# Kernel tuning notes

Hardware: AMD Instinct MI355X
Metric: run time of the kernel (lower is better)

The kernel has to match this reference:

```python
import jax, jax.numpy as jnp
import numpy as np

B, S, D, H = 4, 4096, 1024, 1024


def log_g(x):
    # where(x >= 0, log(relu(x) + 0.5), -softplus(-x)); relu(x)+0.5 >= 0.5 so log is safe
    return jnp.where(x >= 0, jnp.log(jax.nn.relu(x) + 0.5), -jax.nn.softplus(-x))


def setup_inputs() -> dict:
    key = jax.random.key(0)
    ks = jax.random.split(key, 8)
    scale = 1.0 / np.sqrt(D)
    return {
        "x_t": jax.random.normal(ks[0], (B, S, D), dtype=jnp.float32),
        "pre_h": jax.random.normal(ks[1], (B, 1, H), dtype=jnp.float32),
        "W_f": jax.random.uniform(ks[2], (H, D), jnp.float32, -scale, scale),
        "b_f": jax.random.uniform(ks[3], (H,), jnp.float32, -scale, scale),
        "W_i": jax.random.uniform(ks[4], (H, D), jnp.float32, -scale, scale),
        "b_i": jax.random.uniform(ks[5], (H,), jnp.float32, -scale, scale),
        "W_h": jax.random.uniform(ks[6], (H, D), jnp.float32, -scale, scale),
        "b_h": jax.random.uniform(ks[7], (H,), jnp.float32, -scale, scale),
    }


def reference(x_t, pre_h, W_f, b_f, W_i, b_i, W_h, b_h):
    sp = jax.nn.softplus
    f_pre = jnp.einsum("bsd,hd->bsh", x_t, W_f) + b_f
    i_pre = jnp.einsum("bsd,hd->bsh", x_t, W_i) + b_i
    h_pre = jnp.einsum("bsd,hd->bsh", x_t, W_h) + b_h

    diff = sp(-f_pre) - sp(-i_pre)
    log_f = -sp(diff)        # (B, S, H)
    log_i = -sp(-diff)       # (B, S, H)

    log_h0 = log_g(pre_h)                 # (B, 1, H)
    log_tilde_h = log_g(h_pre)            # (B, S, H)
    log_values = jnp.concatenate([log_h0, log_i + log_tilde_h], axis=1)  # (B, S+1, H)

    # parallel_scan_log: pad cumsum at END of seq dim (as in source: F.pad(..., (0,0,0,1)))
    a_star = jnp.pad(jnp.cumsum(log_f, axis=1), ((0, 0), (0, 1), (0, 0)))  # (B, S+1, H)
    log_h0_plus_b_star = jax.lax.cumlogsumexp(log_values - a_star, axis=1)
    log_h = a_star + log_h0_plus_b_star
    return jnp.exp(log_h)[:, 1:]  # (B, S, H)
```

## Files before the change

kernel.cpp:

```cpp
#include <hip/hip_runtime.h>
#include <hip/hip_bf16.h>
#include <math.h>

#define B_DIM 4
#define S_DIM 4096
#define K_DIM 1024
#define H_DIM 1024
#define M_DIM (B_DIM * S_DIM)

#define BMT 128
#define BNT 128
#define KT_ITERS (K_DIM / 32)

#define NCHUNK 64
#define CLEN (S_DIM / NCHUNK)

typedef __attribute__((ext_vector_type(8))) _Float16 f16x8;
typedef __attribute__((ext_vector_type(4))) _Float16 f16x4;
typedef __attribute__((ext_vector_type(4))) float f32x4;

__device__ __forceinline__ float sp_f(float x) {
    return fmaxf(x, 0.0f) + __logf(1.0f + __expf(-fabsf(x)));
}
__device__ __forceinline__ float log_g_f(float x) {
    return (x >= 0.0f) ? __logf(x + 0.5f) : -sp_f(-x);
}
__device__ __forceinline__ float logaddexp_f(float a, float b) {
    float m = fmaxf(a, b);
    return m + __logf(1.0f + __expf(-fabsf(a - b)));
}
__device__ __forceinline__ float exp_sat(float x) {
    return __expf(fminf(x, 85.0f));
}

__device__ __forceinline__ void gl_lds16(const void* g, void* l) {
    __builtin_amdgcn_global_load_lds(
        (const __attribute__((address_space(1))) unsigned int*)g,
        (__attribute__((address_space(3))) unsigned int*)l, 16, 0, 0);
}

__global__ __launch_bounds__(256) void conv_f16(
    const float* __restrict__ src, _Float16* __restrict__ dst, int n4)
{
    int i = blockIdx.x * 256 + threadIdx.x;
    if (i >= n4) return;
    float4 v = ((const float4*)src)[i];
    f16x4 o = {(_Float16)v.x, (_Float16)v.y, (_Float16)v.z, (_Float16)v.w};
    ((f16x4*)dst)[i] = o;
}

__global__ __launch_bounds__(512, 2) void gemm3(
    const _Float16* __restrict__ xh,
    const _Float16* __restrict__ wh,
    const float* __restrict__ bfp, const float* __restrict__ bip,
    const float* __restrict__ bhp,
    _Float16* __restrict__ lf_out, _Float16* __restrict__ w_out)
{
    __shared__ __align__(16) char smem0[32768];
    __shared__ __align__(16) char smem1[32768];
    __shared__ __align__(16) char smem2[32768];

    const int tid = threadIdx.x;
    const int lane = tid & 63;
    const int wv = tid >> 6;
    const int wm = wv >> 2;
    const int wn = wv & 3;

    const int row0 = blockIdx.y * BMT;
    const int col0 = blockIdx.x * BNT;

    const int srow = tid >> 2;
    const int sswz = (tid & 3) ^ ((srow >> 1) & 3);
    unsigned ga0 = (unsigned)(((row0 + srow) * K_DIM + sswz * 8) * 2);
    unsigned gb0 = (unsigned)(((0 * H_DIM + col0 + srow) * K_DIM + sswz * 8) * 2);
    unsigned gb1 = (unsigned)(((1 * H_DIM + col0 + srow) * K_DIM + sswz * 8) * 2);
    unsigned gb2 = (unsigned)(((2 * H_DIM + col0 + srow) * K_DIM + sswz * 8) * 2);

    const char* __restrict__ px = (const char*)xh;
    const char* __restrict__ pw = (const char*)wh;

    int aoff[4], boff[2];
#pragma unroll
    for (int mi = 0; mi < 4; ++mi) {
        int ar = wm * 64 + mi * 16 + (lane & 15);
        aoff[mi] = ar * 64 + ((((lane >> 4) ^ ((ar >> 1) & 3))) << 4);
    }
#pragma unroll
    for (int nj = 0; nj < 2; ++nj) {
        int bc = wn * 32 + nj * 16 + (lane & 15);
        boff[nj] = 8192 + bc * 64 + ((((lane >> 4) ^ ((bc >> 1) & 3))) << 4);
    }

    f32x4 acc[3][4][2];
#pragma unroll
    for (int g = 0; g < 3; ++g)
#pragma unroll
        for (int mi = 0; mi < 4; ++mi)
#pragma unroll
            for (int nj = 0; nj < 2; ++nj)
                acc[g][mi][nj] = (f32x4){0.f, 0.f, 0.f, 0.f};

#define STAGE4(S) do { \
    gl_lds16(px + ga0, (S) + tid * 16); \
    gl_lds16(pw + gb0, (S) + 8192  + tid * 16); \
    gl_lds16(pw + gb1, (S) + 16384 + tid * 16); \
    gl_lds16(pw + gb2, (S) + 24576 + tid * 16); \
    ga0 += 64; gb0 += 64; gb1 += 64; gb2 += 64; } while (0)

#define LGKM0 do { \
    asm volatile("s_waitcnt lgkmcnt(0)" ::: "memory"); \
    __builtin_amdgcn_sched_barrier(0); } while (0)

#define MFMA_HALF(A0, A1, MI0, MI1) do { \
    __builtin_amdgcn_s_setprio(1); \
    _Pragma("unroll") \
    for (int g = 0; g < 3; ++g) { \
        acc[g][MI0][0] = __builtin_amdgcn_mfma_f32_16x16x32_f16(A0, b_[g][0], acc[g][MI0][0], 0, 0, 0); \
        acc[g][MI0][1] = __builtin_amdgcn_mfma_f32_16x16x32_f16(A0, b_[g][1], acc[g][MI0][1], 0, 0, 0); \
        acc[g][MI1][0] = __builtin_amdgcn_mfma_f32_16x16x32_f16(A1, b_[g][0], acc[g][MI1][0], 0, 0, 0); \
        acc[g][MI1][1] = __builtin_amdgcn_mfma_f32_16x16x32_f16(A1, b_[g][1], acc[g][MI1][1], 0, 0, 0); \
    } \
    __builtin_amdgcn_s_setprio(0); } while (0)

#define TILE(CUR, STG, DOSTAGE, VN) do { \
    f16x8 a0_ = *(const f16x8*)((CUR) + aoff[0]); \
    f16x8 a1_ = *(const f16x8*)((CUR) + aoff[1]); \
    f16x8 b_[3][2]; \
    _Pragma("unroll") \
    for (int g = 0; g < 3; ++g) { \
        b_[g][0] = *(const f16x8*)((CUR) + g * 8192 + boff[0]); \
        b_[g][1] = *(const f16x8*)((CUR) + g * 8192 + boff[1]); \
    } \
    if (DOSTAGE) { \
        gl_lds16(px + ga0, (STG) + tid * 16); \
        gl_lds16(pw + gb0, (STG) + 8192 + tid * 16); \
    } \
    __builtin_amdgcn_sched_barrier(0); \
    __builtin_amdgcn_s_barrier(); \
    LGKM0; \
    MFMA_HALF(a0_, a1_, 0, 1); \
    __builtin_amdgcn_sched_barrier(0); \
    __builtin_amdgcn_s_barrier(); \
    f16x8 a2_ = *(const f16x8*)((CUR) + aoff[2]); \
    f16x8 a3_ = *(const f16x8*)((CUR) + aoff[3]); \
    if (DOSTAGE) { \
        gl_lds16(pw + gb1, (STG) + 16384 + tid * 16); \
        gl_lds16(pw + gb2, (STG) + 24576 + tid * 16); \
        ga0 += 64; gb0 += 64; gb1 += 64; gb2 += 64; \
    } \
    __builtin_amdgcn_sched_barrier(0); \
    __builtin_amdgcn_s_barrier(); \
    LGKM0; \
    MFMA_HALF(a2_, a3_, 2, 3); \
    asm volatile("s_waitcnt vmcnt(" #VN ")" ::: "memory"); \
    __builtin_amdgcn_sched_barrier(0); \
    __builtin_amdgcn_s_barrier(); } while (0)

    STAGE4(smem0);
    STAGE4(smem1);
    asm volatile("s_waitcnt vmcnt(4)" ::: "memory");
    __builtin_amdgcn_sched_barrier(0);
    __builtin_amdgcn_s_barrier();

#pragma unroll 1
    for (int it = 0; it < 10; ++it) {
        TILE(smem0, smem2, 1, 4);
        TILE(smem1, smem0, 1, 4);
        TILE(smem2, smem1, 1, 4);
    }
    TILE(smem0, smem2, 0, 0);
    TILE(smem1, smem0, 0, 0);

#undef TILE
#undef MFMA_HALF
#undef LGKM0
#undef STAGE4

    int nidx[2];
    float bfv[2], biv[2], bhv[2];
#pragma unroll
    for (int nj = 0; nj < 2; ++nj) {
        nidx[nj] = col0 + wn * 32 + nj * 16 + (lane & 15);
        bfv[nj] = bfp[nidx[nj]];
        biv[nj] = bip[nidx[nj]];
        bhv[nj] = bhp[nidx[nj]];
    }
#pragma unroll
    for (int mi = 0; mi < 4; ++mi) {
#pragma unroll
        for (int r = 0; r < 4; ++r) {
            int m = row0 + wm * 64 + mi * 16 + ((lane >> 4) << 2) + r;
#pragma unroll
            for (int nj = 0; nj < 2; ++nj) {
                float f_pre = acc[0][mi][nj][r] + bfv[nj];
                float i_pre = acc[1][mi][nj][r] + biv[nj];
                float h_pre = acc[2][mi][nj][r] + bhv[nj];
                float diff = sp_f(-f_pre) - sp_f(-i_pre);
                float lfv = -sp_f(diff);
                float wv_ = -sp_f(-diff) + log_g_f(h_pre);
                size_t o = (size_t)m * H_DIM + nidx[nj];
                lf_out[o] = (_Float16)lfv;
                w_out[o] = (_Float16)wv_;
            }
        }
    }
}

__global__ __launch_bounds__(256) void scan_pass_a(
    const _Float16* __restrict__ lf, const _Float16* __restrict__ w,
    float2* __restrict__ agg)
{
    int tid = blockIdx.x * blockDim.x + threadIdx.x;
    int hq = tid & (H_DIM / 4 - 1);
    int b = (tid >> 8) & (B_DIM - 1);
    int q = tid >> 10;
    int h0 = hq * 4;

    int tstart = q * CLEN + 1;
    int tend = (q == NCHUNK - 1) ? (S_DIM - 1) : (q * CLEN + CLEN);

    size_t idx = (size_t)(b * S_DIM + tstart) * H_DIM + h0;
    float c[4] = {0.f, 0.f, 0.f, 0.f};
    float r[4] = {-INFINITY, -INFINITY, -INFINITY, -INFINITY};
#pragma unroll 4
    for (int t = tstart; t <= tend; ++t) {
        f16x4 lv = *(const f16x4*)(lf + idx);
        f16x4 wv = *(const f16x4*)(w + idx - H_DIM);
#pragma unroll
        for (int j = 0; j < 4; ++j) {
            c[j] += (float)lv[j];
            r[j] = logaddexp_f(r[j], (float)wv[j] - c[j]);
        }
        idx += H_DIM;
    }
#pragma unroll
    for (int j = 0; j < 4; ++j)
        agg[(size_t)(b * H_DIM + h0 + j) * NCHUNK + q] = make_float2(c[j], r[j]);
}

__global__ __launch_bounds__(256) void scan_pass_b(
    const _Float16* __restrict__ lf, const float* __restrict__ preh,
    const float2* __restrict__ agg, float2* __restrict__ prefix)
{
    int col = blockIdx.x * blockDim.x + threadIdx.x;
    int h = col & (H_DIM - 1);
    int b = col >> 10;

    float lf0 = (float)lf[(size_t)(b * S_DIM) * H_DIM + h];
    float C = lf0;
    float R = log_g_f(preh[b * H_DIM + h]) - lf0;
    for (int q = 0; q < NCHUNK; ++q) {
        prefix[(size_t)col * NCHUNK + q] = make_float2(C, R);
        float2 a = agg[(size_t)col * NCHUNK + q];
        float Rn = logaddexp_f(R, a.y - C);
        C += a.x;
        R = Rn;
    }
}

__global__ __launch_bounds__(256) void scan_pass_c(
    const _Float16* __restrict__ lf, const _Float16* __restrict__ w,
    const float2* __restrict__ prefix, float* __restrict__ out)
{
    int tid = blockIdx.x * blockDim.x + threadIdx.x;
    int hq = tid & (H_DIM / 4 - 1);
    int b = (tid >> 8) & (B_DIM - 1);
    int q = tid >> 10;
    int h0 = hq * 4;

    float C[4], R[4];
#pragma unroll
    for (int j = 0; j < 4; ++j) {
        float2 p = prefix[(size_t)(b * H_DIM + h0 + j) * NCHUNK + q];
        C[j] = p.x; R[j] = p.y;
    }

    int tstart = q * CLEN + 1;
    int tend = (q == NCHUNK - 1) ? (S_DIM - 1) : (q * CLEN + CLEN);

    size_t idx = (size_t)(b * S_DIM + tstart) * H_DIM + h0;
#pragma unroll 4
    for (int t = tstart; t <= tend; ++t) {
        f16x4 lv = *(const f16x4*)(lf + idx);
        f16x4 wv = *(const f16x4*)(w + idx - H_DIM);
        float4 ov;
        C[0] += (float)lv[0]; R[0] = logaddexp_f(R[0], (float)wv[0] - C[0]); ov.x = exp_sat(C[0] + R[0]);
        C[1] += (float)lv[1]; R[1] = logaddexp_f(R[1], (float)wv[1] - C[1]); ov.y = exp_sat(C[1] + R[1]);
        C[2] += (float)lv[2]; R[2] = logaddexp_f(R[2], (float)wv[2] - C[2]); ov.z = exp_sat(C[2] + R[2]);
        C[3] += (float)lv[3]; R[3] = logaddexp_f(R[3], (float)wv[3] - C[3]); ov.w = exp_sat(C[3] + R[3]);
        *(float4*)(out + idx - H_DIM) = ov;
        idx += H_DIM;
    }
    if (q == NCHUNK - 1) {
        f16x4 wv = *(const f16x4*)(w + idx - H_DIM);
        float4 ov;
        ov.x = exp_sat(logaddexp_f(R[0], (float)wv[0]));
        ov.y = exp_sat(logaddexp_f(R[1], (float)wv[1]));
        ov.z = exp_sat(logaddexp_f(R[2], (float)wv[2]));
        ov.w = exp_sat(logaddexp_f(R[3], (float)wv[3]));
        *(float4*)(out + idx - H_DIM) = ov;
    }
}

extern "C" void kernel_launch(void* const* d_in, const int* in_sizes, int n_in,
                              void* d_out, int out_size, void* d_ws, size_t ws_size,
                              hipStream_t stream) {
    const float* x    = (const float*)d_in[0];
    const float* preh = (const float*)d_in[1];
    const float* Wf   = (const float*)d_in[2];
    const float* bf   = (const float*)d_in[3];
    const float* Wi   = (const float*)d_in[4];
    const float* bi   = (const float*)d_in[5];
    const float* Wh   = (const float*)d_in[6];
    const float* bh   = (const float*)d_in[7];
    float* out = (float*)d_out;

    _Float16* xh = (_Float16*)d_ws;
    _Float16* wh = xh + (size_t)M_DIM * K_DIM;
    _Float16* lf = wh + (size_t)3 * H_DIM * K_DIM;
    _Float16* wbuf = lf + (size_t)M_DIM * H_DIM;
    float2* agg = (float2*)(wbuf + (size_t)M_DIM * H_DIM);
    float2* prefix = agg + (size_t)B_DIM * H_DIM * NCHUNK;

    conv_f16<<<(M_DIM * K_DIM / 4) / 256, 256, 0, stream>>>(x, xh, M_DIM * K_DIM / 4);
    conv_f16<<<(H_DIM * K_DIM / 4) / 256, 256, 0, stream>>>(Wf, wh, H_DIM * K_DIM / 4);
    conv_f16<<<(H_DIM * K_DIM / 4) / 256, 256, 0, stream>>>(
        Wi, wh + (size_t)H_DIM * K_DIM, H_DIM * K_DIM / 4);
    conv_f16<<<(H_DIM * K_DIM / 4) / 256, 256, 0, stream>>>(
        Wh, wh + (size_t)2 * H_DIM * K_DIM, H_DIM * K_DIM / 4);

    gemm3<<<dim3(H_DIM / BNT, M_DIM / BMT), 512, 0, stream>>>(
        xh, wh, bf, bi, bh, lf, wbuf);

    scan_pass_a<<<(B_DIM * H_DIM * NCHUNK / 4) / 256, 256, 0, stream>>>(lf, wbuf, agg);
    scan_pass_b<<<(B_DIM * H_DIM) / 256, 256, 0, stream>>>(lf, preh, agg, prefix);
    scan_pass_c<<<(B_DIM * H_DIM * NCHUNK / 4) / 256, 256, 0, stream>>>(lf, wbuf, prefix, out);
}
```

Before: 369.3 us.

## Enlarge GEMM row tile to 256, merge conversions, parallelize prefix scan pass

Doubles the GEMM M tile from 128 to 256 rows, so each wave now covers 128 rows with 8 MFMA row fragments. This is meant to reuse each staged weight tile across more rows and cut weight traffic, with A staging split into two 128-row loads per K step. It also merges the four fp32-to-fp16 conversion launches into one kernel, and replaces the serial 64-step chunk-prefix loop in scan_pass_b with a wavefront shuffle-based log-space scan. The trade-off is a larger footprint: the accumulator array doubles and LDS grows to 120KB per block, which conflicts with the launch bound of two 512-thread blocks per CU and risks register spills or lower occupancy.

```diff
diff --git a/kernel.cpp b/kernel.cpp
--- a/kernel.cpp
+++ b/kernel.cpp
@@ -8,7 +8,7 @@
 #define H_DIM 1024
 #define M_DIM (B_DIM * S_DIM)
 
-#define BMT 128
+#define BMT 256
 #define BNT 128
 #define KT_ITERS (K_DIM / 32)
 
@@ -39,14 +39,29 @@
         (__attribute__((address_space(3))) unsigned int*)l, 16, 0, 0);
 }
 
-__global__ __launch_bounds__(256) void conv_f16(
-    const float* __restrict__ src, _Float16* __restrict__ dst, int n4)
+#define NX_F4 (M_DIM * K_DIM / 4)
+#define NW_F4 (H_DIM * K_DIM / 4)
+__global__ __launch_bounds__(256) void conv_all(
+    const float* __restrict__ x, const float* __restrict__ Wf,
+    const float* __restrict__ Wi, const float* __restrict__ Wh,
+    _Float16* __restrict__ xh, _Float16* __restrict__ wh)
 {
     int i = blockIdx.x * 256 + threadIdx.x;
-    if (i >= n4) return;
-    float4 v = ((const float4*)src)[i];
+    const float* src;
+    _Float16* dst;
+    int j;
+    if (i < NX_F4) {
+        src = x; dst = xh; j = i;
+    } else {
+        int t = i - NX_F4;
+        int g = t >> 18;
+        j = t & (NW_F4 - 1);
+        src = (g == 0) ? Wf : (g == 1) ? Wi : Wh;
+        dst = wh + (size_t)g * H_DIM * K_DIM;
+    }
+    float4 v = ((const float4*)src)[j];
     f16x4 o = {(_Float16)v.x, (_Float16)v.y, (_Float16)v.z, (_Float16)v.w};
-    ((f16x4*)dst)[i] = o;
+    ((f16x4*)dst)[j] = o;
 }
 
 __global__ __launch_bounds__(512, 2) void gemm3(
@@ -56,9 +71,9 @@
     const float* __restrict__ bhp,
     _Float16* __restrict__ lf_out, _Float16* __restrict__ w_out)
 {
-    __shared__ __align__(16) char smem0[32768];
-    __shared__ __align__(16) char smem1[32768];
-    __shared__ __align__(16) char smem2[32768];
+    __shared__ __align__(16) char smem0[40960];
+    __shared__ __align__(16) char smem1[40960];
+    __shared__ __align__(16) char smem2[40960];
 
     const int tid = threadIdx.x;
     const int lane = tid & 63;
@@ -69,49 +84,47 @@
     const int row0 = blockIdx.y * BMT;
     const int col0 = blockIdx.x * BNT;
 
-    const int srow = tid >> 2;
-    const int sswz = (tid & 3) ^ ((srow >> 1) & 3);
-    unsigned ga0 = (unsigned)(((row0 + srow) * K_DIM + sswz * 8) * 2);
-    unsigned gb0 = (unsigned)(((0 * H_DIM + col0 + srow) * K_DIM + sswz * 8) * 2);
-    unsigned gb1 = (unsigned)(((1 * H_DIM + col0 + srow) * K_DIM + sswz * 8) * 2);
-    unsigned gb2 = (unsigned)(((2 * H_DIM + col0 + srow) * K_DIM + sswz * 8) * 2);
+    const int sswz = (tid & 3) ^ ((tid >> 3) & 3);
+    unsigned ga0 = (unsigned)(((row0 + (tid >> 2)) * K_DIM + sswz * 8) * 2);
+    unsigned ga1 = ga0 + 128 * K_DIM * 2;
+    unsigned gb0 = (unsigned)(((0 * H_DIM + col0 + (tid >> 2)) * K_DIM + sswz * 8) * 2);
+    unsigned gb1 = (unsigned)(((1 * H_DIM + col0 + (tid >> 2)) * K_DIM + sswz * 8) * 2);
+    unsigned gb2 = (unsigned)(((2 * H_DIM + col0 + (tid >> 2)) * K_DIM + sswz * 8) * 2);
 
     const char* __restrict__ px = (const char*)xh;
     const char* __restrict__ pw = (const char*)wh;
 
-    int aoff[4], boff[2];
-#pragma unroll
-    for (int mi = 0; mi < 4; ++mi) {
-        int ar = wm * 64 + mi * 16 + (lane & 15);
-        aoff[mi] = ar * 64 + ((((lane >> 4) ^ ((ar >> 1) & 3))) << 4);
-    }
-#pragma unroll
-    for (int nj = 0; nj < 2; ++nj) {
-        int bc = wn * 32 + nj * 16 + (lane & 15);
-        boff[nj] = 8192 + bc * 64 + ((((lane >> 4) ^ ((bc >> 1) & 3))) << 4);
-    }
-
-    f32x4 acc[3][4][2];
+    const int ar = wm * 128 + (lane & 15);
+    const int aoff0 = ar * 64 + ((((lane >> 4) ^ ((ar >> 1) & 3))) << 4);
+    const int bc = wn * 32 + (lane & 15);
+    const int boff0 = 16384 + bc * 64 + ((((lane >> 4) ^ ((bc >> 1) & 3))) << 4);
+
+    f32x4 acc[3][8][2];
 #pragma unroll
     for (int g = 0; g < 3; ++g)
 #pragma unroll
-        for (int mi = 0; mi < 4; ++mi)
+        for (int mi = 0; mi < 8; ++mi)
 #pragma unroll
             for (int nj = 0; nj < 2; ++nj)
                 acc[g][mi][nj] = (f32x4){0.f, 0.f, 0.f, 0.f};
 
-#define STAGE4(S) do { \
+#define STAGE5(S) do { \
     gl_lds16(px + ga0, (S) + tid * 16); \
-    gl_lds16(pw + gb0, (S) + 8192  + tid * 16); \
-    gl_lds16(pw + gb1, (S) + 16384 + tid * 16); \
-    gl_lds16(pw + gb2, (S) + 24576 + tid * 16); \
-    ga0 += 64; gb0 += 64; gb1 += 64; gb2 += 64; } while (0)
+    gl_lds16(px + ga1, (S) + 8192 + tid * 16); \
+    gl_lds16(pw + gb0, (S) + 16384 + tid * 16); \
+    gl_lds16(pw + gb1, (S) + 24576 + tid * 16); \
+    gl_lds16(pw + gb2, (S) + 32768 + tid * 16); \
+    ga0 += 64; ga1 += 64; gb0 += 64; gb1 += 64; gb2 += 64; } while (0)
+
+#define SBAR do { \
+    __builtin_amdgcn_sched_barrier(0); \
+    __builtin_amdgcn_s_barrier(); } while (0)
 
 #define LGKM0 do { \
     asm volatile("s_waitcnt lgkmcnt(0)" ::: "memory"); \
     __builtin_amdgcn_sched_barrier(0); } while (0)
 
-#define MFMA_HALF(A0, A1, MI0, MI1) do { \
+#define MFMA12(A0, A1, MI0, MI1) do { \
     __builtin_amdgcn_s_setprio(1); \
     _Pragma("unroll") \
     for (int g = 0; g < 3; ++g) { \
@@ -123,58 +136,60 @@
     __builtin_amdgcn_s_setprio(0); } while (0)
 
 #define TILE(CUR, STG, DOSTAGE, VN) do { \
-    f16x8 a0_ = *(const f16x8*)((CUR) + aoff[0]); \
-    f16x8 a1_ = *(const f16x8*)((CUR) + aoff[1]); \
     f16x8 b_[3][2]; \
     _Pragma("unroll") \
     for (int g = 0; g < 3; ++g) { \
-        b_[g][0] = *(const f16x8*)((CUR) + g * 8192 + boff[0]); \
-        b_[g][1] = *(const f16x8*)((CUR) + g * 8192 + boff[1]); \
+        b_[g][0] = *(const f16x8*)((CUR) + g * 8192 + boff0); \
+        b_[g][1] = *(const f16x8*)((CUR) + g * 8192 + boff0 + 1024); \
     } \
+    f16x8 a0_ = *(const f16x8*)((CUR) + aoff0); \
+    f16x8 a1_ = *(const f16x8*)((CUR) + aoff0 + 1024); \
     if (DOSTAGE) { \
         gl_lds16(px + ga0, (STG) + tid * 16); \
-        gl_lds16(pw + gb0, (STG) + 8192 + tid * 16); \
+        gl_lds16(px + ga1, (STG) + 8192 + tid * 16); \
     } \
-    __builtin_amdgcn_sched_barrier(0); \
-    __builtin_amdgcn_s_barrier(); \
-    LGKM0; \
-    MFMA_HALF(a0_, a1_, 0, 1); \
-    __builtin_amdgcn_sched_barrier(0); \
-    __builtin_amdgcn_s_barrier(); \
-    f16x8 a2_ = *(const f16x8*)((CUR) + aoff[2]); \
-    f16x8 a3_ = *(const f16x8*)((CUR) + aoff[3]); \
+    SBAR; LGKM0; \
+    MFMA12(a0_, a1_, 0, 1); \
+    f16x8 a2_ = *(const f16x8*)((CUR) + aoff0 + 2048); \
+    f16x8 a3_ = *(const f16x8*)((CUR) + aoff0 + 3072); \
+    if (DOSTAGE) gl_lds16(pw + gb0, (STG) + 16384 + tid * 16); \
+    SBAR; LGKM0; \
+    MFMA12(a2_, a3_, 2, 3); \
+    f16x8 a4_ = *(const f16x8*)((CUR) + aoff0 + 4096); \
+    f16x8 a5_ = *(const f16x8*)((CUR) + aoff0 + 5120); \
+    if (DOSTAGE) gl_lds16(pw + gb1, (STG) + 24576 + tid * 16); \
+    SBAR; LGKM0; \
+    MFMA12(a4_, a5_, 4, 5); \
+    f16x8 a6_ = *(const f16x8*)((CUR) + aoff0 + 6144); \
+    f16x8 a7_ = *(const f16x8*)((CUR) + aoff0 + 7168); \
     if (DOSTAGE) { \
-        gl_lds16(pw + gb1, (STG) + 16384 + tid * 16); \
-        gl_lds16(pw + gb2, (STG) + 24576 + tid * 16); \
-        ga0 += 64; gb0 += 64; gb1 += 64; gb2 += 64; \
+        gl_lds16(pw + gb2, (STG) + 32768 + tid * 16); \
+        ga0 += 64; ga1 += 64; gb0 += 64; gb1 += 64; gb2 += 64; \
     } \
-    __builtin_amdgcn_sched_barrier(0); \
-    __builtin_amdgcn_s_barrier(); \
-    LGKM0; \
-    MFMA_HALF(a2_, a3_, 2, 3); \
+    SBAR; LGKM0; \
+    MFMA12(a6_, a7_, 6, 7); \
     asm volatile("s_waitcnt vmcnt(" #VN ")" ::: "memory"); \
-    __builtin_amdgcn_sched_barrier(0); \
-    __builtin_amdgcn_s_barrier(); } while (0)
-
-    STAGE4(smem0);
-    STAGE4(smem1);
-    asm volatile("s_waitcnt vmcnt(4)" ::: "memory");
-    __builtin_amdgcn_sched_barrier(0);
-    __builtin_amdgcn_s_barrier();
+    SBAR; } while (0)
+
+    STAGE5(smem0);
+    STAGE5(smem1);
+    asm volatile("s_waitcnt vmcnt(5)" ::: "memory");
+    SBAR;
 
 #pragma unroll 1
     for (int it = 0; it < 10; ++it) {
-        TILE(smem0, smem2, 1, 4);
-        TILE(smem1, smem0, 1, 4);
-        TILE(smem2, smem1, 1, 4);
+        TILE(smem0, smem2, 1, 5);
+        TILE(smem1, smem0, 1, 5);
+        TILE(smem2, smem1, 1, 5);
     }
     TILE(smem0, smem2, 0, 0);
     TILE(smem1, smem0, 0, 0);
 
 #undef TILE
-#undef MFMA_HALF
+#undef MFMA12
 #undef LGKM0
-#undef STAGE4
+#undef SBAR
+#undef STAGE5
 
     int nidx[2];
     float bfv[2], biv[2], bhv[2];
@@ -186,10 +201,10 @@
         bhv[nj] = bhp[nidx[nj]];
     }
 #pragma unroll
-    for (int mi = 0; mi < 4; ++mi) {
+    for (int mi = 0; mi < 8; ++mi) {
 #pragma unroll
         for (int r = 0; r < 4; ++r) {
-            int m = row0 + wm * 64 + mi * 16 + ((lane >> 4) << 2) + r;
+            int m = row0 + wm * 128 + mi * 16 + ((lane >> 4) << 2) + r;
 #pragma unroll
             for (int nj = 0; nj < 2; ++nj) {
                 float f_pre = acc[0][mi][nj][r] + bfv[nj];
@@ -242,20 +257,30 @@
     const _Float16* __restrict__ lf, const float* __restrict__ preh,
     const float2* __restrict__ agg, float2* __restrict__ prefix)
 {
-    int col = blockIdx.x * blockDim.x + threadIdx.x;
+    int lane = threadIdx.x & 63;
+    int col = blockIdx.x * 4 + (threadIdx.x >> 6);
     int h = col & (H_DIM - 1);
     int b = col >> 10;
 
+    float2 a = agg[(size_t)col * NCHUNK + lane];
+    float c = a.x, r = a.y;
+#pragma unroll
+    for (int off = 1; off < 64; off <<= 1) {
+        float pc = __shfl_up(c, off, 64);
+        float pr = __shfl_up(r, off, 64);
+        if (lane >= off) {
+            r = logaddexp_f(pr, r - pc);
+            c = pc + c;
+        }
+    }
+    float ec = __shfl_up(c, 1, 64);
+    float er = __shfl_up(r, 1, 64);
+    if (lane == 0) { ec = 0.0f; er = -INFINITY; }
     float lf0 = (float)lf[(size_t)(b * S_DIM) * H_DIM + h];
-    float C = lf0;
-    float R = log_g_f(preh[b * H_DIM + h]) - lf0;
-    for (int q = 0; q < NCHUNK; ++q) {
-        prefix[(size_t)col * NCHUNK + q] = make_float2(C, R);
-        float2 a = agg[(size_t)col * NCHUNK + q];
-        float Rn = logaddexp_f(R, a.y - C);
-        C += a.x;
-        R = Rn;
-    }
+    float C0 = lf0;
+    float R0 = log_g_f(preh[b * H_DIM + h]) - lf0;
+    prefix[(size_t)col * NCHUNK + lane] =
+        make_float2(C0 + ec, logaddexp_f(R0, er - C0));
 }
 
 __global__ __launch_bounds__(256) void scan_pass_c(
@@ -322,17 +347,12 @@
     float2* agg = (float2*)(wbuf + (size_t)M_DIM * H_DIM);
     float2* prefix = agg + (size_t)B_DIM * H_DIM * NCHUNK;
 
-    conv_f16<<<(M_DIM * K_DIM / 4) / 256, 256, 0, stream>>>(x, xh, M_DIM * K_DIM / 4);
-    conv_f16<<<(H_DIM * K_DIM / 4) / 256, 256, 0, stream>>>(Wf, wh, H_DIM * K_DIM / 4);
-    conv_f16<<<(H_DIM * K_DIM / 4) / 256, 256, 0, stream>>>(
-        Wi, wh + (size_t)H_DIM * K_DIM, H_DIM * K_DIM / 4);
-    conv_f16<<<(H_DIM * K_DIM / 4) / 256, 256, 0, stream>>>(
-        Wh, wh + (size_t)2 * H_DIM * K_DIM, H_DIM * K_DIM / 4);
+    conv_all<<<(NX_F4 + 3 * NW_F4) / 256, 256, 0, stream>>>(x, Wf, Wi, Wh, xh, wh);
 
     gemm3<<<dim3(H_DIM / BNT, M_DIM / BMT), 512, 0, stream>>>(
         xh, wh, bf, bi, bh, lf, wbuf);
 
     scan_pass_a<<<(B_DIM * H_DIM * NCHUNK / 4) / 256, 256, 0, stream>>>(lf, wbuf, agg);
-    scan_pass_b<<<(B_DIM * H_DIM) / 256, 256, 0, stream>>>(lf, preh, agg, prefix);
+    scan_pass_b<<<(B_DIM * H_DIM) / 4, 256, 0, stream>>>(lf, preh, agg, prefix);
     scan_pass_c<<<(B_DIM * H_DIM * NCHUNK / 4) / 256, 256, 0, stream>>>(lf, wbuf, prefix, out);
 }
```

Result: faster. 322.8 us, median of 3 (-12.6%).
